# Performance work log

Measured on AMD Instinct MI355X. Metric: run time of the kernel, lower is better.

## Reference

```python
import jax, jax.numpy as jnp
import numpy as np

NUM_FREQ = 4
MAX_FREQ_LOG2 = 10.0
# standard NeRF frequency bands: 2^linspace(0, max_freq_log2, num_freq)
FREQ_BANDS = 2.0 ** np.linspace(0.0, MAX_FREQ_LOG2, NUM_FREQ).astype(np.float32)


def positional_encoding(x):
    # x: [N, 3] -> [N, 3*(1 + 2*num_freq)] = [N, 27]
    xf = x[..., None, :] * jnp.asarray(FREQ_BANDS, dtype=x.dtype)[:, None]  # [N, F, 3]
    enc = jnp.concatenate([jnp.sin(xf), jnp.cos(xf)], axis=-1)  # [N, F, 6]
    return jnp.concatenate([x, enc.reshape(x.shape[0], -1)], axis=-1)


def setup_inputs() -> dict:
    key = jax.random.key(0)
    k1, k2, k3 = jax.random.split(key, 3)
    N = 2097152
    x = jax.random.normal(k1, (N, 3), dtype=jnp.float32)
    in_dim, hidden = 27, 32
    # torch Linear default init scale ~ 1/sqrt(fan_in)
    W1 = jax.random.normal(k2, (in_dim, hidden), dtype=jnp.float32) / np.sqrt(in_dim)
    b1 = jnp.zeros((hidden,), dtype=jnp.float32)
    W2 = jax.random.normal(k3, (hidden, 1), dtype=jnp.float32) / np.sqrt(hidden)
    b2 = jnp.zeros((1,), dtype=jnp.float32)
    return {"x": x, "W1": W1, "b1": b1, "W2": W2, "b2": b2}


def reference(x, W1, b1, W2, b2):
    t = positional_encoding(x)                    # [N, 27]
    h = jax.nn.relu(t @ W1 + b1)                  # [N, 32]
    out = jax.nn.relu(h @ W2 + b2)                # [N, 1]
    return out
```

## Files before the change

### kernel.cpp

```cpp
#include <hip/hip_runtime.h>


#define NPTS  2097152
#define BLOCK 256
#define TILES 4
#define NBLK  (NPTS / (BLOCK * TILES))

typedef __bf16 bf16x8 __attribute__((ext_vector_type(8)));
typedef float  f32x4  __attribute__((ext_vector_type(4)));
typedef float  f32x2  __attribute__((ext_vector_type(2)));

__global__ __launch_bounds__(BLOCK, 8) void nerf_mfma6(
    const float* __restrict__ x,
    const float* __restrict__ W1,
    const float* __restrict__ b1,
    const float* __restrict__ W2,
    const float* __restrict__ b2,
    float* __restrict__ out)
{
    const int tid  = threadIdx.x;
    const int wave = tid >> 6;
    const int lane = tid & 63;
    const int g    = lane >> 4;
    const int c    = lane & 15;

    const float INV2PI = 0.15915494309189535f;
    float Fg = 1.0f;
    Fg = (g == 1) ? 10.079368f : Fg;
    Fg = (g == 2) ? 101.59367f : Fg;
    Fg = (g == 3) ? 1024.0f    : Fg;
    Fg *= INV2PI;

    bf16x8 afrag[2];
    #pragma unroll
    for (int mt = 0; mt < 2; ++mt) {
        const int j = mt * 16 + c;
        #pragma unroll
        for (int i = 0; i < 3; ++i)
            afrag[mt][i] = (__bf16)W1[(3 + 6 * g + i) * 32 + j];
        #pragma unroll
        for (int i = 3; i < 6; ++i)
            afrag[mt][i] = (__bf16)W1[(6 + 6 * g + (i - 3)) * 32 + j];
        afrag[mt][6] = (__bf16)((g < 3) ? W1[g * 32 + j] : b1[j]);
        afrag[mt][7] = (__bf16)0.0f;
    }

    f32x2 w2p[2][2];
    #pragma unroll
    for (int mt = 0; mt < 2; ++mt)
        #pragma unroll
        for (int rr = 0; rr < 2; ++rr) {
            w2p[mt][rr][0] = W2[mt * 16 + g * 4 + 2 * rr + 0];
            w2p[mt][rr][1] = W2[mt * 16 + g * 4 + 2 * rr + 1];
        }
    const float bias2 = b2[0];

    const int tbase = blockIdx.x * (4 * TILES) + wave * TILES;

    #pragma unroll
    for (int t = 0; t < TILES; ++t) {
        const float* xb = x + (size_t)(tbase + t) * 192;
        float px[4][3];
        #pragma unroll
        for (int nt = 0; nt < 4; ++nt)
            #pragma unroll
            for (int cm = 0; cm < 3; ++cm)
                px[nt][cm] = xb[(16 * nt + c) * 3 + cm];

        float p[4];
        #pragma unroll
        for (int nt = 0; nt < 4; ++nt) {
            const float x0 = px[nt][0], x1 = px[nt][1], x2 = px[nt][2];

            const float a0 = __builtin_amdgcn_fractf(x0 * Fg);
            const float a1 = __builtin_amdgcn_fractf(x1 * Fg);
            const float a2 = __builtin_amdgcn_fractf(x2 * Fg);
            float extra = x0;
            extra = (g == 1) ? x1 : extra;
            extra = (g == 2) ? x2 : extra;
            extra = (g == 3) ? 1.0f : extra;

            bf16x8 bf;
            bf[0] = (__bf16)__builtin_amdgcn_sinf(a0);
            bf[1] = (__bf16)__builtin_amdgcn_sinf(a1);
            bf[2] = (__bf16)__builtin_amdgcn_sinf(a2);
            bf[3] = (__bf16)__builtin_amdgcn_cosf(a0);
            bf[4] = (__bf16)__builtin_amdgcn_cosf(a1);
            bf[5] = (__bf16)__builtin_amdgcn_cosf(a2);
            bf[6] = (__bf16)extra;
            bf[7] = (__bf16)0.0f;

            f32x4 acc0 = {0.f, 0.f, 0.f, 0.f};
            f32x4 acc1 = {0.f, 0.f, 0.f, 0.f};
            acc0 = __builtin_amdgcn_mfma_f32_16x16x32_bf16(afrag[0], bf, acc0, 0, 0, 0);
            acc1 = __builtin_amdgcn_mfma_f32_16x16x32_bf16(afrag[1], bf, acc1, 0, 0, 0);

            f32x2 ps = {0.0f, 0.0f};
            #pragma unroll
            for (int rr = 0; rr < 2; ++rr) {
                f32x2 a;
                a[0] = fmaxf(acc0[2 * rr + 0], 0.0f);
                a[1] = fmaxf(acc0[2 * rr + 1], 0.0f);
                ps = ps + a * w2p[0][rr];
                f32x2 b;
                b[0] = fmaxf(acc1[2 * rr + 0], 0.0f);
                b[1] = fmaxf(acc1[2 * rr + 1], 0.0f);
                ps = ps + b * w2p[1][rr];
            }
            p[nt] = ps[0] + ps[1];
        }

        const bool hi2 = (g >= 2), odd = (g & 1);
        const float s0 = hi2 ? p[0] : p[2];
        const float s1 = hi2 ? p[1] : p[3];
        const float k0 = hi2 ? p[2] : p[0];
        const float k1 = hi2 ? p[3] : p[1];
        const float r0 = k0 + __shfl_xor(s0, 32, 64);
        const float r1 = k1 + __shfl_xor(s1, 32, 64);
        const float uk = odd ? r1 : r0;
        const float us = odd ? r0 : r1;
        const float S  = uk + __shfl_xor(us, 16, 64);

        out[(size_t)(tbase + t) * 64 + lane] = fmaxf(S + bias2, 0.0f);
    }
}

extern "C" void kernel_launch(void* const* d_in, const int* in_sizes, int n_in,
                              void* d_out, int out_size, void* d_ws, size_t ws_size,
                              hipStream_t stream) {
    const float* x  = (const float*)d_in[0];
    const float* W1 = (const float*)d_in[1];
    const float* b1 = (const float*)d_in[2];
    const float* W2 = (const float*)d_in[3];
    const float* b2 = (const float*)d_in[4];
    float* out = (float*)d_out;

    nerf_mfma6<<<NBLK, BLOCK, 0, stream>>>(x, W1, b1, W2, b2, out);
}
```

Before: 19.88 us.

## Compute second layer with a bf16 MFMA instead of FMAs and cross-lane shuffles

Packs the ReLU'd hidden activations into a bf16 vector and runs the 32-to-1 output projection as a third MFMA, with W2 held in the A fragment. This drops the per-lane fp32 multiply-adds and the two shuffle-based reductions, and the final output is picked from the MFMA result with lane-group selects. It also loads x as float3 instead of scalar loads. The trade-off is extra rounding, since hidden activations and W2 are now bf16. It also spends one more matrix op per point group, and most rows of that 16-wide MFMA are unused.

New measurement: 19.96 us. No clear change (+0.4%).

```diff
diff --git a/kernel.cpp b/kernel.cpp
--- a/kernel.cpp
+++ b/kernel.cpp
@@ -8,9 +8,8 @@
 
 typedef __bf16 bf16x8 __attribute__((ext_vector_type(8)));
 typedef float  f32x4  __attribute__((ext_vector_type(4)));
-typedef float  f32x2  __attribute__((ext_vector_type(2)));
 
-__global__ __launch_bounds__(BLOCK, 8) void nerf_mfma6(
+__global__ __launch_bounds__(BLOCK, 8) void nerf_mfma7(
     const float* __restrict__ x,
     const float* __restrict__ W1,
     const float* __restrict__ b1,
@@ -45,36 +44,31 @@
         afrag[mt][7] = (__bf16)0.0f;
     }
 
-    f32x2 w2p[2][2];
+    bf16x8 a2;
     #pragma unroll
-    for (int mt = 0; mt < 2; ++mt)
-        #pragma unroll
-        for (int rr = 0; rr < 2; ++rr) {
-            w2p[mt][rr][0] = W2[mt * 16 + g * 4 + 2 * rr + 0];
-            w2p[mt][rr][1] = W2[mt * 16 + g * 4 + 2 * rr + 1];
-        }
+    for (int i = 0; i < 4; ++i) {
+        a2[i]     = (__bf16)W2[4 * g + i];
+        a2[4 + i] = (__bf16)W2[16 + 4 * g + i];
+    }
     const float bias2 = b2[0];
 
     const int tbase = blockIdx.x * (4 * TILES) + wave * TILES;
 
     #pragma unroll
     for (int t = 0; t < TILES; ++t) {
-        const float* xb = x + (size_t)(tbase + t) * 192;
-        float px[4][3];
+        const float3* xb3 = (const float3*)(x + (size_t)(tbase + t) * 192);
+        float3 P[4];
         #pragma unroll
-        for (int nt = 0; nt < 4; ++nt)
-            #pragma unroll
-            for (int cm = 0; cm < 3; ++cm)
-                px[nt][cm] = xb[(16 * nt + c) * 3 + cm];
+        for (int nt = 0; nt < 4; ++nt) P[nt] = xb3[16 * nt + c];
 
         float p[4];
         #pragma unroll
         for (int nt = 0; nt < 4; ++nt) {
-            const float x0 = px[nt][0], x1 = px[nt][1], x2 = px[nt][2];
+            const float x0 = P[nt].x, x1 = P[nt].y, x2 = P[nt].z;
 
             const float a0 = __builtin_amdgcn_fractf(x0 * Fg);
             const float a1 = __builtin_amdgcn_fractf(x1 * Fg);
-            const float a2 = __builtin_amdgcn_fractf(x2 * Fg);
+            const float a2f = __builtin_amdgcn_fractf(x2 * Fg);
             float extra = x0;
             extra = (g == 1) ? x1 : extra;
             extra = (g == 2) ? x2 : extra;
@@ -83,10 +77,10 @@
             bf16x8 bf;
             bf[0] = (__bf16)__builtin_amdgcn_sinf(a0);
             bf[1] = (__bf16)__builtin_amdgcn_sinf(a1);
-            bf[2] = (__bf16)__builtin_amdgcn_sinf(a2);
+            bf[2] = (__bf16)__builtin_amdgcn_sinf(a2f);
             bf[3] = (__bf16)__builtin_amdgcn_cosf(a0);
             bf[4] = (__bf16)__builtin_amdgcn_cosf(a1);
-            bf[5] = (__bf16)__builtin_amdgcn_cosf(a2);
+            bf[5] = (__bf16)__builtin_amdgcn_cosf(a2f);
             bf[6] = (__bf16)extra;
             bf[7] = (__bf16)0.0f;
 
@@ -95,33 +89,22 @@
             acc0 = __builtin_amdgcn_mfma_f32_16x16x32_bf16(afrag[0], bf, acc0, 0, 0, 0);
             acc1 = __builtin_amdgcn_mfma_f32_16x16x32_bf16(afrag[1], bf, acc1, 0, 0, 0);
 
-            f32x2 ps = {0.0f, 0.0f};
+            bf16x8 h8;
             #pragma unroll
-            for (int rr = 0; rr < 2; ++rr) {
-                f32x2 a;
-                a[0] = fmaxf(acc0[2 * rr + 0], 0.0f);
-                a[1] = fmaxf(acc0[2 * rr + 1], 0.0f);
-                ps = ps + a * w2p[0][rr];
-                f32x2 b;
-                b[0] = fmaxf(acc1[2 * rr + 0], 0.0f);
-                b[1] = fmaxf(acc1[2 * rr + 1], 0.0f);
-                ps = ps + b * w2p[1][rr];
+            for (int r = 0; r < 4; ++r) {
+                h8[r]     = (__bf16)fmaxf(acc0[r], 0.0f);
+                h8[4 + r] = (__bf16)fmaxf(acc1[r], 0.0f);
             }
-            p[nt] = ps[0] + ps[1];
+            f32x4 o = {0.f, 0.f, 0.f, 0.f};
+            o = __builtin_amdgcn_mfma_f32_16x16x32_bf16(a2, h8, o, 0, 0, 0);
+            p[nt] = o[0];
         }
 
-        const bool hi2 = (g >= 2), odd = (g & 1);
-        const float s0 = hi2 ? p[0] : p[2];
-        const float s1 = hi2 ? p[1] : p[3];
-        const float k0 = hi2 ? p[2] : p[0];
-        const float k1 = hi2 ? p[3] : p[1];
-        const float r0 = k0 + __shfl_xor(s0, 32, 64);
-        const float r1 = k1 + __shfl_xor(s1, 32, 64);
-        const float uk = odd ? r1 : r0;
-        const float us = odd ? r0 : r1;
-        const float S  = uk + __shfl_xor(us, 16, 64);
-
-        out[(size_t)(tbase + t) * 64 + lane] = fmaxf(S + bias2, 0.0f);
+        float v = p[0];
+        v = (g == 1) ? p[1] : v;
+        v = (g == 2) ? p[2] : v;
+        v = (g == 3) ? p[3] : v;
+        out[(size_t)(tbase + t) * 64 + lane] = fmaxf(v + bias2, 0.0f);
     }
 }
 
@@ -135,5 +118,5 @@
     const float* b2 = (const float*)d_in[4];
     float* out = (float*)d_out;
 
-    nerf_mfma6<<<NBLK, BLOCK, 0, stream>>>(x, W1, b1, W2, b2, out);
+    nerf_mfma7<<<NBLK, BLOCK, 0, stream>>>(x, W1, b1, W2, b2, out);
 }
```
